# Kernel tuning notes

Measured on AMD Instinct MI355X. Metric: run time of the kernel, lower is better.

The kernel has to match this reference:

```python
import jax, jax.numpy as jnp
import numpy as np

N = 100000   # nodes
E = 600000   # directed edges
F = 128      # input feature dim (input_size)
K = 2        # hops
OUT = 64     # output_size
NEG_SLOPE = 0.2  # GAT leaky-relu slope


def setup_inputs() -> dict:
    key = jax.random.key(0)
    ks = jax.random.split(key, 8)
    feature = jax.random.normal(ks[0], (N, F), dtype=jnp.float32)
    edge_index = jax.random.randint(ks[1], (2, E), 0, N)
    # attention vectors (heads=1): separate params per direction, shared over hops
    att_f_src = jax.random.normal(ks[2], (F,), dtype=jnp.float32) * 0.1
    att_f_dst = jax.random.normal(ks[3], (F,), dtype=jnp.float32) * 0.1
    att_r_src = jax.random.normal(ks[4], (F,), dtype=jnp.float32) * 0.1
    att_r_dst = jax.random.normal(ks[5], (F,), dtype=jnp.float32) * 0.1
    # final dense: in = input_size * 2 * (K+1)
    W = jax.random.normal(ks[6], (2 * (K + 1) * F, OUT), dtype=jnp.float32) * 0.05
    b = jnp.zeros((OUT,), dtype=jnp.float32)
    return {"feature": feature, "edge_index": edge_index,
            "att_f_src": att_f_src, "att_f_dst": att_f_dst,
            "att_r_src": att_r_src, "att_r_dst": att_r_dst,
            "W": W, "b": b}


def _propagate(x, src, dst, a_src, a_dst, n):
    """K hops of GAT-style attention aggregation along src->dst edges.
    Returns [h0, h1, ..., hK], each [n, F]. No feature transform (heads=1, concat=False)."""
    outs = [x]
    h = x
    for _ in range(K):
        s = h @ a_src                     # [n]
        d = h @ a_dst                     # [n]
        e = jax.nn.leaky_relu(s[src] + d[dst], NEG_SLOPE)   # [E]
        # segment softmax over incoming edges of each dst node
        m = jax.ops.segment_max(e, dst, num_segments=n)
        m = jnp.where(jnp.isfinite(m), m, 0.0)              # empty segments -> 0
        ee = jnp.exp(e - m[dst])
        denom = jax.ops.segment_sum(ee, dst, num_segments=n)
        alpha = ee / (denom[dst] + 1e-16)                   # [E]
        h = jax.ops.segment_sum(alpha[:, None] * h[src], dst, num_segments=n)  # [n,F]
        outs.append(h)
    return outs


def reference(feature, edge_index, att_f_src, att_f_dst, att_r_src, att_r_dst, W, b):
    src, dst = edge_index[0], edge_index[1]
    outs_fwd = _propagate(feature, src, dst, att_f_src, att_f_dst, N)   # forward edges
    outs_rev = _propagate(feature, dst, src, att_r_src, att_r_dst, N)   # reversed edges
    h = jnp.concatenate(outs_fwd + outs_rev, axis=-1)   # [N, 2*(K+1)*F]
    return h @ W + b
```

## Files before the change

kernel.cpp:

```cpp
#include <hip/hip_runtime.h>
#include <math.h>

#define F 128
#define OUTDIM 64
#define NEG 0.2f

typedef __attribute__((ext_vector_type(8))) short bf16x8;
typedef __attribute__((ext_vector_type(4))) float f32x4;

__device__ __forceinline__ float blo(unsigned u) { return __uint_as_float(u << 16); }
__device__ __forceinline__ float bhi(unsigned u) { return __uint_as_float(u & 0xFFFF0000u); }
__device__ __forceinline__ unsigned bpack(float a, float b) {
    unsigned ua = __float_as_uint(a), ub = __float_as_uint(b);
    ua += 0x7FFFu + ((ua >> 16) & 1u);
    ub += 0x7FFFu + ((ub >> 16) & 1u);
    return (ua >> 16) | (ub & 0xFFFF0000u);
}

__global__ void zero_ints(int* __restrict__ p, int n) {
    int i = blockIdx.x * blockDim.x + threadIdx.x;
    if (i < n) p[i] = 0;
}

__global__ void hist_kernel(const int* __restrict__ src, const int* __restrict__ dst,
                            int* __restrict__ degF, int* __restrict__ degR,
                            int* __restrict__ rankF, int* __restrict__ rankR, int E) {
    int e = blockIdx.x * blockDim.x + threadIdx.x;
    if (e < E) {
        rankF[e] = atomicAdd(&degF[dst[e]], 1);
        rankR[e] = atomicAdd(&degR[src[e]], 1);
    }
}

__global__ void scan_pass1(const int* __restrict__ degF, const int* __restrict__ degR,
                           int* __restrict__ rsF, int* __restrict__ rsR,
                           int* __restrict__ bsums, int N) {
    const int arr = blockIdx.y;
    const int* deg = arr ? degR : degF;
    int* rs = arr ? rsR : rsF;
    int tid = threadIdx.x;
    int base = blockIdx.x * 1024 + tid * 4;
    int v[4];
#pragma unroll
    for (int i = 0; i < 4; i++) v[i] = (base + i < N) ? deg[base + i] : 0;
    int s1 = v[0] + v[1] + v[2] + v[3];
    __shared__ int sd[256];
    sd[tid] = s1;
    __syncthreads();
    for (int off = 1; off < 256; off <<= 1) {
        int t = (tid >= off) ? sd[tid - off] : 0;
        __syncthreads();
        sd[tid] += t;
        __syncthreads();
    }
    int run = sd[tid] - s1;
#pragma unroll
    for (int i = 0; i < 4; i++) {
        run += v[i];
        if (base + i < N) rs[base + i + 1] = run;
    }
    if (tid == 255) bsums[arr * 128 + blockIdx.x] = sd[255];
    if (tid == 0 && blockIdx.x == 0) rs[0] = 0;
}

__global__ void scan_pass2(int* __restrict__ bsums, int nb) {
    int arr = blockIdx.y;
    int tid = threadIdx.x;
    __shared__ int sd[128];
    int v = (tid < nb) ? bsums[arr * 128 + tid] : 0;
    sd[tid] = v;
    __syncthreads();
    for (int off = 1; off < 128; off <<= 1) {
        int t = (tid >= off) ? sd[tid - off] : 0;
        __syncthreads();
        sd[tid] += t;
        __syncthreads();
    }
    bsums[arr * 128 + tid] = sd[tid];
}

__global__ void scan_pass3(int* __restrict__ rsF, int* __restrict__ rsR,
                           const int* __restrict__ bsums, int N) {
    int arr = blockIdx.y;
    if (blockIdx.x == 0) return;
    int* rs = arr ? rsR : rsF;
    int off = bsums[arr * 128 + blockIdx.x - 1];
    int base = blockIdx.x * 1024 + threadIdx.x * 4;
#pragma unroll
    for (int i = 0; i < 4; i++)
        if (base + i < N) rs[base + i + 1] += off;
}

__global__ void scatter_kernel(const int* __restrict__ src, const int* __restrict__ dst,
                               const int* __restrict__ rsF, const int* __restrict__ rsR,
                               const int* __restrict__ rankF, const int* __restrict__ rankR,
                               int* __restrict__ colF, int* __restrict__ colR, int E) {
    int e = blockIdx.x * blockDim.x + threadIdx.x;
    if (e < E) {
        int s = src[e], d = dst[e];
        colF[rsF[d] + rankF[e]] = s;
        colR[rsR[s] + rankR[e]] = d;
    }
}

__global__ void sd4_kernel(const float* __restrict__ x,
                           const float* __restrict__ af_s, const float* __restrict__ af_d,
                           const float* __restrict__ ar_s, const float* __restrict__ ar_d,
                           float* __restrict__ sf, float* __restrict__ df,
                           float* __restrict__ sr, float* __restrict__ dr,
                           unsigned* __restrict__ xbf, int N) {
    int node = blockIdx.x * 4 + (threadIdx.x >> 6);
    int lane = threadIdx.x & 63;
    if (node >= N) return;
    const float2 xv = *(const float2*)&x[(size_t)node * F + 2 * lane];
    xbf[(size_t)node * 64 + lane] = bpack(xv.x, xv.y);
    float2 a;
    a = *(const float2*)&af_s[2 * lane]; float vsf = xv.x * a.x + xv.y * a.y;
    a = *(const float2*)&af_d[2 * lane]; float vdf = xv.x * a.x + xv.y * a.y;
    a = *(const float2*)&ar_s[2 * lane]; float vsr = xv.x * a.x + xv.y * a.y;
    a = *(const float2*)&ar_d[2 * lane]; float vdr = xv.x * a.x + xv.y * a.y;
#pragma unroll
    for (int off = 32; off > 0; off >>= 1) {
        vsf += __shfl_xor(vsf, off);
        vdf += __shfl_xor(vdf, off);
        vsr += __shfl_xor(vsr, off);
        vdr += __shfl_xor(vdr, off);
    }
    if (lane == 0) { sf[node] = vsf; df[node] = vdf; sr[node] = vsr; dr[node] = vdr; }
}

struct AggDir {
    const unsigned* hin_bf;
    const float* s;
    const float* d;
    const int* rs;
    const int* col;
    unsigned* hout_bf;
    const float* a_s;
    const float* a_d;
    float* s_out;
    float* d_out;
};

__global__ __launch_bounds__(256) void agg_kernel(AggDir D0, AggDir D1, int N) {
    AggDir P = blockIdx.y ? D1 : D0;
    int node = blockIdx.x * 16 + (threadIdx.x >> 4);
    int lane = threadIdx.x & 15;
    int qbase = threadIdx.x & 48;
    if (node >= N) return;
    float di = P.d[node];
    int beg = P.rs[node], end = P.rs[node + 1];
    int deg = end - beg;
    float m = -INFINITY, l = 0.f;
    float4 a0 = make_float4(0.f, 0.f, 0.f, 0.f);
    float4 a1 = make_float4(0.f, 0.f, 0.f, 0.f);

    for (int base = 0; base < deg; base += 16) {
        int cnt = min(16, deg - base);
        int sj_l = 0;
        float e_l = -INFINITY;
        if (lane < cnt) {
            sj_l = P.col[beg + base + lane];
            float e = P.s[sj_l] + di;
            e_l = (e >= 0.f) ? e : NEG * e;
        }
        float bm = e_l;
#pragma unroll
        for (int off = 8; off > 0; off >>= 1) bm = fmaxf(bm, __shfl_xor(bm, off));
        float nm = fmaxf(m, bm);
        float p_l = (lane < cnt) ? __expf(e_l - nm) : 0.f;
        float ps = p_l;
#pragma unroll
        for (int off = 8; off > 0; off >>= 1) ps += __shfl_xor(ps, off);
        float sc = (m == -INFINITY) ? 0.f : __expf(m - nm);
        l = l * sc + ps;
        a0.x *= sc; a0.y *= sc; a0.z *= sc; a0.w *= sc;
        a1.x *= sc; a1.y *= sc; a1.z *= sc; a1.w *= sc;
        for (int j0 = 0; j0 < cnt; j0 += 8) {
            int sj[8]; float p[8]; uint4 hb[8];
#pragma unroll
            for (int u = 0; u < 8; u++) {
                sj[u] = __shfl(sj_l, qbase + j0 + u);
                p[u]  = __shfl(p_l,  qbase + j0 + u);
            }
#pragma unroll
            for (int u = 0; u < 8; u++) {
                if (j0 + u < cnt) {
                    hb[u] = *(const uint4*)&P.hin_bf[(size_t)sj[u] * 64 + 4 * lane];
                } else {
                    hb[u] = make_uint4(0u, 0u, 0u, 0u);
                }
            }
#pragma unroll
            for (int u = 0; u < 8; u++) {
                a0.x += p[u] * blo(hb[u].x); a0.y += p[u] * bhi(hb[u].x);
                a0.z += p[u] * blo(hb[u].y); a0.w += p[u] * bhi(hb[u].y);
                a1.x += p[u] * blo(hb[u].z); a1.y += p[u] * bhi(hb[u].z);
                a1.z += p[u] * blo(hb[u].w); a1.w += p[u] * bhi(hb[u].w);
            }
        }
        m = nm;
    }

    float4 o0, o1;
    if (deg > 0) {
        float inv = 1.f / (l + 1e-16f);
        o0.x = a0.x * inv; o0.y = a0.y * inv; o0.z = a0.z * inv; o0.w = a0.w * inv;
        o1.x = a1.x * inv; o1.y = a1.y * inv; o1.z = a1.z * inv; o1.w = a1.w * inv;
    } else {
        o0 = make_float4(0.f, 0.f, 0.f, 0.f);
        o1 = o0;
    }
    uint4 hb;
    hb.x = bpack(o0.x, o0.y); hb.y = bpack(o0.z, o0.w);
    hb.z = bpack(o1.x, o1.y); hb.w = bpack(o1.z, o1.w);
    *(uint4*)&P.hout_bf[(size_t)node * 64 + 4 * lane] = hb;
    if (P.a_s) {
        float4 b0, b1;
        b0 = *(const float4*)&P.a_s[8 * lane];
        b1 = *(const float4*)&P.a_s[8 * lane + 4];
        float vs = o0.x * b0.x + o0.y * b0.y + o0.z * b0.z + o0.w * b0.w
                 + o1.x * b1.x + o1.y * b1.y + o1.z * b1.z + o1.w * b1.w;
        b0 = *(const float4*)&P.a_d[8 * lane];
        b1 = *(const float4*)&P.a_d[8 * lane + 4];
        float vd = o0.x * b0.x + o0.y * b0.y + o0.z * b0.z + o0.w * b0.w
                 + o1.x * b1.x + o1.y * b1.y + o1.z * b1.z + o1.w * b1.w;
#pragma unroll
        for (int off = 8; off > 0; off >>= 1) {
            vs += __shfl_xor(vs, off);
            vd += __shfl_xor(vd, off);
        }
        if (lane == 0) { P.s_out[node] = vs; P.d_out[node] = vd; }
    }
}

__global__ void wefft_kernel(const float* __restrict__ W, unsigned short* __restrict__ Wt) {
    int i = blockIdx.x * blockDim.x + threadIdx.x;
    if (i >= 64 * 640) return;
    int n = i / 640, k = i % 640;
    float v;
    if (k < 128)      v = W[k * 64 + n] + W[(k + 384) * 64 + n];
    else if (k < 384) v = W[k * 64 + n];
    else              v = W[(k + 128) * 64 + n];
    Wt[(size_t)n * 640 + k] = (unsigned short)(bpack(v, 0.f) & 0xFFFFu);
}

__global__ __launch_bounds__(256) void gemm_mfma(
    const unsigned* __restrict__ XBF, const unsigned* __restrict__ H1FB,
    const unsigned* __restrict__ H2FB, const unsigned* __restrict__ H1RB,
    const unsigned* __restrict__ H2RB,
    const unsigned short* __restrict__ Wt,
    const float* __restrict__ bias, float* __restrict__ out, int N) {
    int wid = threadIdx.x >> 6;
    int lane = threadIdx.x & 63;
    int r = lane & 15;
    int kg = lane >> 4;
    int rowBase = blockIdx.x * 128 + wid * 32;
    int arow0 = rowBase + r;
    int arow1 = rowBase + 16 + r;
    f32x4 acc[2][4];
#pragma unroll
    for (int m = 0; m < 2; m++)
#pragma unroll
        for (int c = 0; c < 4; c++) acc[m][c] = (f32x4){0.f, 0.f, 0.f, 0.f};
    const bf16x8 zro = (bf16x8){0, 0, 0, 0, 0, 0, 0, 0};

#define PANEL(XP, KOFF)                                                          \
    {                                                                            \
        const unsigned short* xsrc = (const unsigned short*)(XP);                \
        _Pragma("unroll")                                                        \
        for (int tt = 0; tt < 4; ++tt) {                                         \
            int kb = tt * 32 + kg * 8;                                           \
            bf16x8 a0 = (arow0 < N) ? *(const bf16x8*)(xsrc + (size_t)arow0 * 128 + kb) : zro; \
            bf16x8 a1 = (arow1 < N) ? *(const bf16x8*)(xsrc + (size_t)arow1 * 128 + kb) : zro; \
            _Pragma("unroll")                                                    \
            for (int c = 0; c < 4; c++) {                                        \
                bf16x8 b = *(const bf16x8*)(Wt + (size_t)(c * 16 + r) * 640 + (KOFF) + kb); \
                acc[0][c] = __builtin_amdgcn_mfma_f32_16x16x32_bf16(a0, b, acc[0][c], 0, 0, 0); \
                acc[1][c] = __builtin_amdgcn_mfma_f32_16x16x32_bf16(a1, b, acc[1][c], 0, 0, 0); \
            }                                                                    \
        }                                                                        \
    }

    PANEL(XBF, 0)
    PANEL(H1FB, 128)
    PANEL(H2FB, 256)
    PANEL(H1RB, 384)
    PANEL(H2RB, 512)
#undef PANEL

#pragma unroll
    for (int m = 0; m < 2; m++)
#pragma unroll
        for (int c = 0; c < 4; c++) {
            int col = c * 16 + r;
            float bv = bias[col];
#pragma unroll
            for (int q = 0; q < 4; q++) {
                int row = rowBase + m * 16 + kg * 4 + q;
                if (row < N) out[(size_t)row * 64 + col] = acc[m][c][q] + bv;
            }
        }
}

extern "C" void kernel_launch(void* const* d_in, const int* in_sizes, int n_in,
                              void* d_out, int out_size, void* d_ws, size_t ws_size,
                              hipStream_t stream) {
    const float* feature = (const float*)d_in[0];
    const int*   eidx    = (const int*)d_in[1];
    const float* af_s    = (const float*)d_in[2];
    const float* af_d    = (const float*)d_in[3];
    const float* ar_s    = (const float*)d_in[4];
    const float* ar_d    = (const float*)d_in[5];
    const float* W       = (const float*)d_in[6];
    const float* bias    = (const float*)d_in[7];
    float* out = (float*)d_out;
    const int N = in_sizes[0] / F;
    const int E = in_sizes[1] / 2;
    const int* src = eidx;
    const int* dst = eidx + E;

    char* ws = (char*)d_ws;
    size_t off = 0;
    auto alloc = [&](size_t b) { size_t r = off; off = (off + b + 255) & ~(size_t)255; return r; };
    unsigned* xbf  = (unsigned*)(ws + alloc((size_t)N * 64 * 4));
    unsigned* h1fb = (unsigned*)(ws + alloc((size_t)N * 64 * 4));
    unsigned* h1rb = (unsigned*)(ws + alloc((size_t)N * 64 * 4));
    unsigned* h2fb = (unsigned*)(ws + alloc((size_t)N * 64 * 4));
    unsigned* h2rb = (unsigned*)(ws + alloc((size_t)N * 64 * 4));
    int*   rsF   = (int*)(ws + alloc((size_t)(N + 1) * 4));
    int*   rsR   = (int*)(ws + alloc((size_t)(N + 1) * 4));
    int*   colF  = (int*)(ws + alloc((size_t)E * 4));
    int*   colR  = (int*)(ws + alloc((size_t)E * 4));
    int*   rankF = (int*)(ws + alloc((size_t)E * 4));
    int*   rankR = (int*)(ws + alloc((size_t)E * 4));
    int*   ints2 = (int*)(ws + alloc((size_t)2 * N * 4));
    int *degF = ints2, *degR = ints2 + N;
    float* fls8 = (float*)(ws + alloc((size_t)8 * N * 4));
    float *sf = fls8, *df = fls8 + N, *sr = fls8 + 2 * (size_t)N, *dr = fls8 + 3 * (size_t)N;
    float *s2f = fls8 + 4 * (size_t)N, *d2f = fls8 + 5 * (size_t)N;
    float *s2r = fls8 + 6 * (size_t)N, *d2r = fls8 + 7 * (size_t)N;
    int*   bsums = (int*)(ws + alloc(256 * 4));
    unsigned short* WeffT = (unsigned short*)(ws + alloc(64 * 640 * 2));

    const int nb = (N + 1023) / 1024;
    zero_ints<<<(2 * N + 255) / 256, 256, 0, stream>>>(ints2, 2 * N);
    hist_kernel<<<(E + 255) / 256, 256, 0, stream>>>(src, dst, degF, degR, rankF, rankR, E);
    scan_pass1<<<dim3(nb, 2), 256, 0, stream>>>(degF, degR, rsF, rsR, bsums, N);
    scan_pass2<<<dim3(1, 2), 128, 0, stream>>>(bsums, nb);
    scan_pass3<<<dim3(nb, 2), 256, 0, stream>>>(rsF, rsR, bsums, N);
    scatter_kernel<<<(E + 255) / 256, 256, 0, stream>>>(src, dst, rsF, rsR, rankF, rankR,
                                                        colF, colR, E);
    sd4_kernel<<<(N + 3) / 4, 256, 0, stream>>>(feature, af_s, af_d, ar_s, ar_d,
                                                sf, df, sr, dr, xbf, N);

    AggDir F1{xbf, sf, df, rsF, colF, h1fb, af_s, af_d, s2f, d2f};
    AggDir R1{xbf, sr, dr, rsR, colR, h1rb, ar_s, ar_d, s2r, d2r};
    agg_kernel<<<dim3((N + 15) / 16, 2), 256, 0, stream>>>(F1, R1, N);
    AggDir F2{h1fb, s2f, d2f, rsF, colF, h2fb, nullptr, nullptr, nullptr, nullptr};
    AggDir R2{h1rb, s2r, d2r, rsR, colR, h2rb, nullptr, nullptr, nullptr, nullptr};
    agg_kernel<<<dim3((N + 15) / 16, 2), 256, 0, stream>>>(F2, R2, N);

    wefft_kernel<<<(64 * 640 + 255) / 256, 256, 0, stream>>>(W, WeffT);
    gemm_mfma<<<(N + 127) / 128, 256, 0, stream>>>(xbf, h1fb, h2fb, h1rb, h2rb,
                                                   WeffT, bias, out, N);
}
```

Measured before the change: 284.1 us.

## Stage GEMM A and W panels through swizzled LDS via direct global-to-LDS loads

```diff
diff --git a/kernel.cpp b/kernel.cpp
--- a/kernel.cpp
+++ b/kernel.cpp
@@ -15,6 +15,12 @@
     ua += 0x7FFFu + ((ua >> 16) & 1u);
     ub += 0x7FFFu + ((ub >> 16) & 1u);
     return (ua >> 16) | (ub & 0xFFFF0000u);
+}
+
+__device__ __forceinline__ void gld_lds16(const void* g, void* l) {
+    __builtin_amdgcn_global_load_lds(
+        (const __attribute__((address_space(1))) unsigned*)g,
+        (__attribute__((address_space(3))) unsigned*)l, 16, 0, 0);
 }
 
 __global__ void zero_ints(int* __restrict__ p, int n) {
@@ -251,35 +257,57 @@
     const unsigned* __restrict__ H2RB,
     const unsigned short* __restrict__ Wt,
     const float* __restrict__ bias, float* __restrict__ out, int N) {
-    int wid = threadIdx.x >> 6;
-    int lane = threadIdx.x & 63;
+    __shared__ unsigned Asm[8192];
+    __shared__ unsigned Bsm[4096];
+    int tid = threadIdx.x;
+    int wid = tid >> 6;
+    int lane = tid & 63;
     int r = lane & 15;
     int kg = lane >> 4;
-    int rowBase = blockIdx.x * 128 + wid * 32;
-    int arow0 = rowBase + r;
-    int arow1 = rowBase + 16 + r;
+    int rowBase = blockIdx.x * 128;
+    int rl0 = wid * 32 + r;
+    int rl1 = rl0 + 16;
+    const int xw = (r & 7) << 4;
     f32x4 acc[2][4];
 #pragma unroll
     for (int m = 0; m < 2; m++)
 #pragma unroll
         for (int c = 0; c < 4; c++) acc[m][c] = (f32x4){0.f, 0.f, 0.f, 0.f};
-    const bf16x8 zro = (bf16x8){0, 0, 0, 0, 0, 0, 0, 0};
-
-#define PANEL(XP, KOFF)                                                          \
+
+#define PANEL(SRC, KOFF)                                                         \
     {                                                                            \
-        const unsigned short* xsrc = (const unsigned short*)(XP);                \
+        const char* asrc = (const char*)(SRC);                                   \
+        const char* bsrc = (const char*)Wt + (size_t)(KOFF) * 2;                 \
+        _Pragma("unroll")                                                        \
+        for (int i = 0; i < 8; ++i) {                                            \
+            int o = wid * 8192 + i * 1024 + (lane << 4);                         \
+            int rowl = o >> 8, colb = o & 255;                                   \
+            int scol = colb ^ ((rowl & 7) << 4);                                 \
+            gld_lds16(asrc + (size_t)(rowBase + rowl) * 256 + scol,              \
+                      &Asm[(wid * 8192 + i * 1024) >> 2]);                       \
+        }                                                                        \
+        _Pragma("unroll")                                                        \
+        for (int i = 0; i < 4; ++i) {                                            \
+            int o = wid * 4096 + i * 1024 + (lane << 4);                         \
+            int rowl = o >> 8, colb = o & 255;                                   \
+            int scol = colb ^ ((rowl & 7) << 4);                                 \
+            gld_lds16(bsrc + (size_t)rowl * 1280 + scol,                         \
+                      &Bsm[(wid * 4096 + i * 1024) >> 2]);                       \
+        }                                                                        \
+        __syncthreads();                                                         \
         _Pragma("unroll")                                                        \
         for (int tt = 0; tt < 4; ++tt) {                                         \
-            int kb = tt * 32 + kg * 8;                                           \
-            bf16x8 a0 = (arow0 < N) ? *(const bf16x8*)(xsrc + (size_t)arow0 * 128 + kb) : zro; \
-            bf16x8 a1 = (arow1 < N) ? *(const bf16x8*)(xsrc + (size_t)arow1 * 128 + kb) : zro; \
+            int colb = tt * 64 + kg * 16;                                        \
+            bf16x8 a0 = *(const bf16x8*)((const char*)Asm + rl0 * 256 + (colb ^ xw)); \
+            bf16x8 a1 = *(const bf16x8*)((const char*)Asm + rl1 * 256 + (colb ^ xw)); \
             _Pragma("unroll")                                                    \
             for (int c = 0; c < 4; c++) {                                        \
-                bf16x8 b = *(const bf16x8*)(Wt + (size_t)(c * 16 + r) * 640 + (KOFF) + kb); \
+                bf16x8 b = *(const bf16x8*)((const char*)Bsm + (c * 16 + r) * 256 + (colb ^ xw)); \
                 acc[0][c] = __builtin_amdgcn_mfma_f32_16x16x32_bf16(a0, b, acc[0][c], 0, 0, 0); \
                 acc[1][c] = __builtin_amdgcn_mfma_f32_16x16x32_bf16(a1, b, acc[1][c], 0, 0, 0); \
             }                                                                    \
         }                                                                        \
+        __syncthreads();                                                         \
     }
 
     PANEL(XBF, 0)
@@ -297,7 +325,7 @@
             float bv = bias[col];
 #pragma unroll
             for (int q = 0; q < 4; q++) {
-                int row = rowBase + m * 16 + kg * 4 + q;
+                int row = rowBase + wid * 32 + m * 16 + kg * 4 + q;
                 if (row < N) out[(size_t)row * 64 + col] = acc[m][c][q] + bv;
             }
         }
```

Result: faster. 256.7 us (-9.6%).
